# Kernel optimization log

Measured on AMD Instinct MI355X. Metric: run time of the kernel, lower is better.

## Reference

```python
import jax, jax.numpy as jnp
import numpy as np
from jax import lax

B, C, V, F, K = 4, 4, 262144, 64, 100
EMA_THETA = 0.9
TAU = 0.1


def setup_inputs() -> dict:
    key = jax.random.key(0)
    k1, k2, k3 = jax.random.split(key, 3)
    proba = jax.random.uniform(k1, (B, C, V), dtype=jnp.float32)
    y = jax.random.randint(k2, (B, C, V), 0, 2, dtype=jnp.int32)
    embeddings = jax.random.normal(k3, (B, F, V), dtype=jnp.float32)
    avg_repr = jnp.zeros((1, C, F), dtype=jnp.float32)  # EMA buffer
    return {"proba": proba, "y": y, "embeddings": embeddings, "avg_repr": avg_repr}


def reference(proba, y, embeddings, avg_repr):
    # --- update average class representation (EMA over masked voxel means) ---
    mask = (y > 0).astype(embeddings.dtype)                      # [B,C,V]
    class_sum = jnp.einsum("bfv,bcv->cf", embeddings, mask)      # [C,F]
    count = jnp.sum(mask, axis=(0, 2))                           # [C]
    mean = class_sum / jnp.maximum(count, 1.0)[:, None]          # [C,F]
    # original: avg*(1-theta) + mean*theta, only for classes with >0 voxels
    avg_new = jnp.where(
        (count > 0)[None, :, None],
        avg_repr * (1.0 - EMA_THETA) + mean[None] * EMA_THETA,
        avg_repr,
    )                                                            # [1,C,F]

    # --- hard example mining: top-k of prod over class probs per voxel ---
    weights = jnp.prod(proba, axis=1)                            # [B,V]
    _, idx = lax.top_k(weights, K)                               # [B,K]
    emb_bvF = jnp.transpose(embeddings, (0, 2, 1))               # [B,V,F]
    he = jnp.take_along_axis(emb_bvF, idx[..., None], axis=1)    # [B,K,F]
    c_map = jnp.argmax(y, axis=1)                                # [B,V] class per voxel
    he_class = jnp.take_along_axis(c_map, idx, axis=1)           # [B,K]

    # --- l_anco: original loop returns on first iteration (class i=0) ---
    i = 0
    nar = avg_new[0, 1:, :]                                      # [C-1,F] (delete class 0)
    # num/(num/neg_den) == neg_den, so out = -log(neg_den) per the source math
    neg_den = jnp.sum(jnp.exp(he[:, :, None, :] * nar[None, None] / TAU), axis=2)  # [B,K,F]
    out = -jnp.log(neg_den)                                      # [B,K,F]
    sel = (he_class == i).astype(out.dtype)                      # [B,K]
    loss = jnp.sum(out, axis=-1) * sel                           # [B,K], masked instead of boolean-select
    return loss
```

## Files before the change

kernel.cpp:

```cpp
#include <hip/hip_runtime.h>

#define B_ 4
#define C_ 4
#define V_ 262144
#define F_ 64
#define K_ 100
#define THETA 0.9f
#define TAU_ 0.1f

typedef unsigned long long ull;


__global__ __launch_bounds__(256) void k_prep(const int* __restrict__ y,
                                              const float* __restrict__ proba,
                                              unsigned short* __restrict__ mask16,
                                              unsigned* __restrict__ cntp,
                                              unsigned short* __restrict__ hist1p,
                                              unsigned* __restrict__ wbits,
                                              float* __restrict__ cs2) {
    __shared__ unsigned lh[256];
    __shared__ unsigned wc[4][2];
    int blk = blockIdx.x;
    int tid = threadIdx.x;
    int wave = tid >> 6, lane = tid & 63;
    int b = blk >> 8;
    int i4 = ((blk & 255) << 8) | tid;

    lh[tid] = 0u;
    if (blk < 8) cs2[(blk << 8) | tid] = 0.f;
    __syncthreads();

    const int4* y1 = (const int4*)(y + ((size_t)(b * C_ + 1)) * V_);
    const int4* y2 = (const int4*)(y + ((size_t)(b * C_ + 2)) * V_);
    const int4* y3 = (const int4*)(y + ((size_t)(b * C_ + 3)) * V_);
    int4 yb = y1[i4], yc = y2[i4], yd = y3[i4];

    unsigned n0 = ((unsigned)(yb.x > 0) << 1) | ((unsigned)(yc.x > 0) << 2) | ((unsigned)(yd.x > 0) << 3);
    unsigned n1 = ((unsigned)(yb.y > 0) << 1) | ((unsigned)(yc.y > 0) << 2) | ((unsigned)(yd.y > 0) << 3);
    unsigned n2 = ((unsigned)(yb.z > 0) << 1) | ((unsigned)(yc.z > 0) << 2) | ((unsigned)(yd.z > 0) << 3);
    unsigned n3 = ((unsigned)(yb.w > 0) << 1) | ((unsigned)(yc.w > 0) << 2) | ((unsigned)(yd.w > 0) << 3);
    mask16[(size_t)b * (V_ / 4) + i4] = (unsigned short)(n0 | (n1 << 4) | (n2 << 8) | (n3 << 12));

    unsigned p12 = ((unsigned)(yb.x > 0) + (yb.y > 0) + (yb.z > 0) + (yb.w > 0))
                 | (((unsigned)(yc.x > 0) + (yc.y > 0) + (yc.z > 0) + (yc.w > 0)) << 16);
    unsigned p3 = (unsigned)(yd.x > 0) + (yd.y > 0) + (yd.z > 0) + (yd.w > 0);
    #pragma unroll
    for (int o = 1; o < 64; o <<= 1) {
        p12 += __shfl_xor(p12, o, 64);
        p3 += __shfl_xor(p3, o, 64);
    }
    if (lane == 0) { wc[wave][0] = p12; wc[wave][1] = p3; }

    const float* p0 = proba + (size_t)(b * C_) * V_;
    float4 qa = ((const float4*)p0)[i4];
    float4 qb = ((const float4*)(p0 + V_))[i4];
    float4 qc = ((const float4*)(p0 + 2 * V_))[i4];
    float4 qd = ((const float4*)(p0 + 3 * V_))[i4];
    uint4 wb;
    wb.x = __float_as_uint(((qa.x * qb.x) * qc.x) * qd.x);
    wb.y = __float_as_uint(((qa.y * qb.y) * qc.y) * qd.y);
    wb.z = __float_as_uint(((qa.z * qb.z) * qc.z) * qd.z);
    wb.w = __float_as_uint(((qa.w * qb.w) * qc.w) * qd.w);
    ((uint4*)wbits)[(size_t)b * (V_ / 4) + i4] = wb;
    atomicAdd(&lh[wb.x >> 24], 1u);
    atomicAdd(&lh[wb.y >> 24], 1u);
    atomicAdd(&lh[wb.z >> 24], 1u);
    atomicAdd(&lh[wb.w >> 24], 1u);
    __syncthreads();

    hist1p[(blk << 8) | tid] = (unsigned short)lh[tid];
    if (tid == 0) {
        unsigned q12 = wc[0][0] + wc[1][0] + wc[2][0] + wc[3][0];
        unsigned q3 = wc[0][1] + wc[1][1] + wc[2][1] + wc[3][1];
        unsigned* o4 = cntp + (blk << 2);
        o4[0] = 0u; o4[1] = q12 & 0xFFFFu;
        o4[2] = q12 >> 16; o4[3] = q3;
    }
}

__global__ __launch_bounds__(256) void k_class_sum(const float* __restrict__ emb,
                                                   const unsigned short* __restrict__ mask16,
                                                   float* __restrict__ cs2,
                                                   const unsigned short* __restrict__ hist1p,
                                                   const unsigned* __restrict__ cntp,
                                                   unsigned* __restrict__ ctrl1,
                                                   float* __restrict__ cnt) {
    __shared__ unsigned short smask[16384];
    __shared__ unsigned bins[256];
    __shared__ float wsum[4][4];
    int blk = blockIdx.x;
    int tid = threadIdx.x;
    int wave = tid >> 6, lane = tid & 63;

    if (blk >= 1024) {
        if (blk < 1028) {
            int b = blk - 1024;
            unsigned s = 0;
            for (int c = 0; c < 256; ++c)
                s += hist1p[(((b << 8) | c) << 8) | tid];
            bins[tid] = s;
            __syncthreads();
            if (wave == 0) {
                int binbase = 255 - 4 * lane;
                unsigned c0 = bins[binbase], c1 = bins[binbase - 1], c2 = bins[binbase - 2], c3 = bins[binbase - 3];
                unsigned cnt4 = c0 + c1 + c2 + c3;
                unsigned pref = cnt4;
                #pragma unroll
                for (int o = 1; o < 64; o <<= 1) {
                    unsigned u = __shfl_up(pref, o, 64);
                    if (lane >= o) pref += u;
                }
                unsigned above = pref - cnt4;
                unsigned t = above;
                int found = -1; unsigned nab = 0;
                if (t + c0 >= K_)                { found = binbase;     nab = t; }
                else if (t + c0 + c1 >= K_)      { found = binbase - 1; nab = t + c0; }
                else if (t + c0 + c1 + c2 >= K_) { found = binbase - 2; nab = t + c0 + c1; }
                else if (t + cnt4 >= K_)         { found = binbase - 3; nab = t + c0 + c1 + c2; }
                if (found >= 0 && above < K_) {
                    ctrl1[b * 2] = (unsigned)found;
                    ctrl1[b * 2 + 1] = nab;
                }
            }
        } else if (wave == 0) {
            unsigned s1 = 0, s2 = 0, s3 = 0;
            #pragma unroll
            for (int r = 0; r < 16; ++r) {
                uint4 p = ((const uint4*)cntp)[(r << 6) | lane];
                s1 += p.y; s2 += p.z; s3 += p.w;
            }
            #pragma unroll
            for (int o = 1; o < 64; o <<= 1) {
                s1 += __shfl_xor(s1, o, 64);
                s2 += __shfl_xor(s2, o, 64);
                s3 += __shfl_xor(s3, o, 64);
            }
            if (lane == 0) {
                cnt[0] = 0.f; cnt[1] = (float)s1;
                cnt[2] = (float)s2; cnt[3] = (float)s3;
            }
        }
        return;
    }

    int s = blk & 3;
    int f = (blk >> 2) & 63;
    int b = blk >> 8;

    {
        const uint4* msrc = (const uint4*)(mask16 + (size_t)b * (V_ / 4) + (s << 14));
        uint4* mdst = (uint4*)smask;
        #pragma unroll
        for (int i = 0; i < 8; ++i) mdst[(i << 8) | tid] = msrc[(i << 8) | tid];
    }
    __syncthreads();

    const float4* ep = (const float4*)emb + ((size_t)((b << 6) | f)) * (V_ / 4) + ((size_t)s << 14);

    float a1 = 0.f, a2 = 0.f, a3 = 0.f;
    for (int o = 0; o < 8; ++o) {
        float4 e[8];
        unsigned mm[8];
        #pragma unroll
        for (int i = 0; i < 8; ++i) e[i] = ep[(((o << 3) | i) << 8) | tid];
        #pragma unroll
        for (int i = 0; i < 8; ++i) mm[i] = smask[(((o << 3) | i) << 8) | tid];
        #pragma unroll
        for (int i = 0; i < 8; ++i) {
            unsigned m = mm[i];
            float4 ev = e[i];
            a1 += ((m >>  1) & 1u ? ev.x : 0.f) + ((m >>  5) & 1u ? ev.y : 0.f)
                + ((m >>  9) & 1u ? ev.z : 0.f) + ((m >> 13) & 1u ? ev.w : 0.f);
            a2 += ((m >>  2) & 1u ? ev.x : 0.f) + ((m >>  6) & 1u ? ev.y : 0.f)
                + ((m >> 10) & 1u ? ev.z : 0.f) + ((m >> 14) & 1u ? ev.w : 0.f);
            a3 += ((m >>  3) & 1u ? ev.x : 0.f) + ((m >>  7) & 1u ? ev.y : 0.f)
                + ((m >> 11) & 1u ? ev.z : 0.f) + ((m >> 15) & 1u ? ev.w : 0.f);
        }
    }
    #pragma unroll
    for (int o = 1; o < 64; o <<= 1) {
        a1 += __shfl_xor(a1, o, 64);
        a2 += __shfl_xor(a2, o, 64);
        a3 += __shfl_xor(a3, o, 64);
    }
    if (lane == 0) { wsum[wave][0] = a1; wsum[wave][1] = a2; wsum[wave][2] = a3; }
    __syncthreads();
    if (tid < 3) {
        float v = wsum[0][tid] + wsum[1][tid] + wsum[2][tid] + wsum[3][tid];
        atomicAdd(&cs2[((blk & 7) << 8) | ((tid + 1) << 6) | f], v);
    }
}

__global__ __launch_bounds__(256) void k_collect(const unsigned* __restrict__ wbits,
                                                 const unsigned* __restrict__ ctrl1,
                                                 unsigned* __restrict__ cntblk,
                                                 unsigned* __restrict__ sbits,
                                                 unsigned* __restrict__ sidx) {
    __shared__ unsigned lcnt;
    int blk = blockIdx.x;
    int b = blk >> 8;
    int cb = blk & 255;
    int tid = threadIdx.x;
    if (tid == 0) lcnt = 0u;
    __syncthreads();
    unsigned T1 = ctrl1[b * 2];
    int base = cb << 10;
    int sb = ((b << 8) | cb) << 6;
    #pragma unroll
    for (int it = 0; it < 4; ++it) {
        int v = base + tid + (it << 8);
        unsigned bits = wbits[(size_t)b * V_ + v];
        if ((bits >> 24) >= T1) {
            unsigned pos = atomicAdd(&lcnt, 1u);
            if (pos < 64u) { sbits[sb | pos] = bits; sidx[sb | pos] = (unsigned)v; }
        }
    }
    __syncthreads();
    if (tid == 0) cntblk[(b << 8) | cb] = (lcnt < 64u) ? lcnt : 64u;
}

#define XSTEP(kk_, k_, j_) { \
    _Pragma("unroll") \
    for (int r = 0; r < 8; ++r) { \
        ull o = __shfl_xor(kk_[r], (j_) >> 3, 64); \
        int p = (lane << 3) | r; \
        bool keepmax = (((p & (k_)) == 0) == ((p & (j_)) == 0)); \
        kk_[r] = (keepmax == (kk_[r] > o)) ? kk_[r] : o; \
    } }
#define LSTEP(kk_, k_, j_) { \
    _Pragma("unroll") \
    for (int r = 0; r < 8; ++r) { \
        if (!(r & (j_))) { \
            int p = (lane << 3) | r; \
            bool up = ((p & (k_)) == 0); \
            ull a = kk_[r], c = kk_[r | (j_)]; \
            ull mx = a > c ? a : c, mn = a > c ? c : a; \
            kk_[r] = up ? mx : mn; \
            kk_[r | (j_)] = up ? mn : mx; \
        } \
    } }

__global__ __launch_bounds__(256) void k_select(const unsigned* __restrict__ ctrl1,
                                                const unsigned* __restrict__ cntblk,
                                                const unsigned* __restrict__ sbits,
                                                const unsigned* __restrict__ sidx,
                                                unsigned* __restrict__ idxout) {
    __shared__ unsigned hist[256];
    __shared__ ull keys[512];
    __shared__ unsigned P16s, fcnt;
    int b = blockIdx.x;
    int tid = threadIdx.x;
    int wave = tid >> 6, lane = tid & 63;
    unsigned T1 = ctrl1[b * 2];
    unsigned nab = ctrl1[b * 2 + 1];

    hist[tid] = 0u;
    keys[tid] = 0ull;
    keys[tid + 256] = 0ull;
    if (tid == 0) fcnt = 0u;
    __syncthreads();

    int c = (int)cntblk[(b << 8) | tid];
    int sb = ((b << 8) | tid) << 6;
    for (int i = 0; i < c; ++i) {
        unsigned bits = sbits[sb | i];
        if ((bits >> 24) == T1) atomicAdd(&hist[(bits >> 16) & 0xFF], 1u);
    }
    __syncthreads();

    if (wave == 0) {
        int binbase = 255 - 4 * lane;
        unsigned c0 = hist[binbase], c1 = hist[binbase - 1], c2 = hist[binbase - 2], c3 = hist[binbase - 3];
        unsigned cnt4 = c0 + c1 + c2 + c3;
        unsigned pref = cnt4;
        #pragma unroll
        for (int o = 1; o < 64; o <<= 1) {
            unsigned u = __shfl_up(pref, o, 64);
            if (lane >= o) pref += u;
        }
        unsigned above = nab + pref - cnt4;
        unsigned t = above;
        int found = -1;
        if (t + c0 >= K_)                { found = binbase;     }
        else if (t + c0 + c1 >= K_)      { found = binbase - 1; }
        else if (t + c0 + c1 + c2 >= K_) { found = binbase - 2; }
        else if (t + cnt4 >= K_)         { found = binbase - 3; }
        if (found >= 0 && above < K_) P16s = (T1 << 8) | (unsigned)found;
    }
    __syncthreads();

    unsigned P16 = P16s;
    for (int i = 0; i < c; ++i) {
        unsigned bits = sbits[sb | i];
        if ((bits >> 16) >= P16) {
            unsigned pos = atomicAdd(&fcnt, 1u);
            if (pos < 512u) keys[pos] = ((ull)bits << 32) | (unsigned)(~sidx[sb | i]);
        }
    }
    __syncthreads();

    if (wave == 0) {
        ull kk[8];
        #pragma unroll
        for (int r = 0; r < 8; ++r) kk[r] = keys[(lane << 3) | r];
        LSTEP(kk, 2, 1)
        LSTEP(kk, 4, 2) LSTEP(kk, 4, 1)
        LSTEP(kk, 8, 4) LSTEP(kk, 8, 2) LSTEP(kk, 8, 1)
        XSTEP(kk, 16, 8) LSTEP(kk, 16, 4) LSTEP(kk, 16, 2) LSTEP(kk, 16, 1)
        XSTEP(kk, 32, 16) XSTEP(kk, 32, 8) LSTEP(kk, 32, 4) LSTEP(kk, 32, 2) LSTEP(kk, 32, 1)
        XSTEP(kk, 64, 32) XSTEP(kk, 64, 16) XSTEP(kk, 64, 8) LSTEP(kk, 64, 4) LSTEP(kk, 64, 2) LSTEP(kk, 64, 1)
        XSTEP(kk, 128, 64) XSTEP(kk, 128, 32) XSTEP(kk, 128, 16) XSTEP(kk, 128, 8) LSTEP(kk, 128, 4) LSTEP(kk, 128, 2) LSTEP(kk, 128, 1)
        XSTEP(kk, 256, 128) XSTEP(kk, 256, 64) XSTEP(kk, 256, 32) XSTEP(kk, 256, 16) XSTEP(kk, 256, 8) LSTEP(kk, 256, 4) LSTEP(kk, 256, 2) LSTEP(kk, 256, 1)
        XSTEP(kk, 512, 256) XSTEP(kk, 512, 128) XSTEP(kk, 512, 64) XSTEP(kk, 512, 32) XSTEP(kk, 512, 16) XSTEP(kk, 512, 8) LSTEP(kk, 512, 4) LSTEP(kk, 512, 2) LSTEP(kk, 512, 1)
        #pragma unroll
        for (int r = 0; r < 8; ++r) {
            int p = (lane << 3) | r;
            if (p < K_) idxout[b * K_ + p] = ~(unsigned)(kk[r] & 0xFFFFFFFFull);
        }
    }
}

__global__ __launch_bounds__(64) void k_final(const float* __restrict__ emb,
                                              const int* __restrict__ y,
                                              const float* __restrict__ avg,
                                              const float* __restrict__ cs2,
                                              const float* __restrict__ cnt,
                                              const unsigned* __restrict__ idxout,
                                              float* __restrict__ out) {
    int blk = blockIdx.x;
    int b = blk / K_;
    int k = blk % K_;
    int lane = threadIdx.x;
    unsigned v = idxout[b * K_ + k];

    float e = emb[((size_t)(b * F_ + lane)) * V_ + v];

    int y0v = y[((size_t)(b * C_ + 0)) * V_ + v];
    int y1v = y[((size_t)(b * C_ + 1)) * V_ + v];
    int y2v = y[((size_t)(b * C_ + 2)) * V_ + v];
    int y3v = y[((size_t)(b * C_ + 3)) * V_ + v];
    int cm = (y0v > 0) ? 0 : ((y1v > 0) ? 1 : ((y2v > 0) ? 2 : ((y3v > 0) ? 3 : 0)));
    float sel = (cm == 0) ? 1.f : 0.f;

    float t = e / TAU_;
    float ssum = 0.f;
    #pragma unroll
    for (int c = 1; c < 4; ++c) {
        float cc = cnt[c];
        float csum = 0.f;
        #pragma unroll
        for (int rep = 0; rep < 8; ++rep) csum += cs2[(rep << 8) | (c << 6) | lane];
        float mean = csum / fmaxf(cc, 1.f);
        float av = avg[c * F_ + lane];
        float nar = (cc > 0.f) ? (av * (1.f - THETA) + mean * THETA) : av;
        ssum += expf(t * nar);
    }
    float term = -logf(ssum);
    #pragma unroll
    for (int o = 32; o > 0; o >>= 1) term += __shfl_down(term, o, 64);
    if (lane == 0) out[b * K_ + k] = term * sel;
}

extern "C" void kernel_launch(void* const* d_in, const int* in_sizes, int n_in,
                              void* d_out, int out_size, void* d_ws, size_t ws_size,
                              hipStream_t stream) {
    const float* proba = (const float*)d_in[0];
    const int* y = (const int*)d_in[1];
    const float* emb = (const float*)d_in[2];
    const float* avg = (const float*)d_in[3];
    float* out = (float*)d_out;

    char* ws = (char*)d_ws;
    float* cs2 = (float*)(ws + 0);
    float* cnt = (float*)(ws + 8192);
    unsigned* ctrl1 = (unsigned*)(ws + 8208);
    unsigned* idxout = (unsigned*)(ws + 8320);
    unsigned* cntp = (unsigned*)(ws + 147456);
    unsigned* cntblk = (unsigned*)(ws + 147456);
    unsigned short* hist1p = (unsigned short*)(ws + 163840);
    unsigned* sbits = (unsigned*)(ws + 163840);
    unsigned* sidx = (unsigned*)(ws + 425984);
    unsigned short* mask16 = (unsigned short*)(ws + 688128);
    unsigned* wbits = (unsigned*)(ws + 1212416);

    k_prep<<<B_ * 256, 256, 0, stream>>>(y, proba, mask16, cntp, hist1p, wbits, cs2);
    k_class_sum<<<1029, 256, 0, stream>>>(emb, mask16, cs2, hist1p, cntp, ctrl1, cnt);
    k_collect<<<B_ * 256, 256, 0, stream>>>(wbits, ctrl1, cntblk, sbits, sidx);
    k_select<<<B_, 256, 0, stream>>>(ctrl1, cntblk, sbits, sidx, idxout);
    k_final<<<B_ * K_, 64, 0, stream>>>(emb, y, avg, cs2, cnt, idxout, out);
}
```

Baseline: 79.06 us.

## Fuse final loss into top-k select kernel and schedule control blocks first

The per-(b,k) final loss kernel is folded into the select kernel. Each of the 4 blocks keeps its top-100 indices in shared memory, and its waves compute 25 losses each with batched gathers, which removes one kernel launch and the idxout round trip. The class_sum kernel's threshold/count control blocks move to the lowest block indices so they get scheduled early, and their histogram loop is unrolled. The cost is that the final stage now runs on only 4 blocks instead of 400, so more serial work falls on each block.

```diff
diff --git a/kernel.cpp b/kernel.cpp
--- a/kernel.cpp
+++ b/kernel.cpp
@@ -92,10 +92,11 @@
     int tid = threadIdx.x;
     int wave = tid >> 6, lane = tid & 63;
 
-    if (blk >= 1024) {
-        if (blk < 1028) {
-            int b = blk - 1024;
+    if (blk < 5) {
+        if (blk < 4) {
+            int b = blk;
             unsigned s = 0;
+            #pragma unroll 8
             for (int c = 0; c < 256; ++c)
                 s += hist1p[(((b << 8) | c) << 8) | tid];
             bins[tid] = s;
@@ -143,9 +144,10 @@
         return;
     }
 
-    int s = blk & 3;
-    int f = (blk >> 2) & 63;
-    int b = blk >> 8;
+    int sblk = blk - 5;
+    int s = sblk & 3;
+    int f = (sblk >> 2) & 63;
+    int b = sblk >> 8;
 
     {
         const uint4* msrc = (const uint4*)(mask16 + (size_t)b * (V_ / 4) + (s << 14));
@@ -187,7 +189,7 @@
     __syncthreads();
     if (tid < 3) {
         float v = wsum[0][tid] + wsum[1][tid] + wsum[2][tid] + wsum[3][tid];
-        atomicAdd(&cs2[((blk & 7) << 8) | ((tid + 1) << 6) | f], v);
+        atomicAdd(&cs2[((sblk & 7) << 8) | ((tid + 1) << 6) | f], v);
     }
 }
 
@@ -244,9 +246,15 @@
                                                 const unsigned* __restrict__ cntblk,
                                                 const unsigned* __restrict__ sbits,
                                                 const unsigned* __restrict__ sidx,
-                                                unsigned* __restrict__ idxout) {
+                                                const float* __restrict__ emb,
+                                                const int* __restrict__ y,
+                                                const float* __restrict__ avg,
+                                                const float* __restrict__ cs2,
+                                                const float* __restrict__ cnt,
+                                                float* __restrict__ out) {
     __shared__ unsigned hist[256];
     __shared__ ull keys[512];
+    __shared__ unsigned topv[112];
     __shared__ unsigned P16s, fcnt;
     int b = blockIdx.x;
     int tid = threadIdx.x;
@@ -315,50 +323,52 @@
         #pragma unroll
         for (int r = 0; r < 8; ++r) {
             int p = (lane << 3) | r;
-            if (p < K_) idxout[b * K_ + p] = ~(unsigned)(kk[r] & 0xFFFFFFFFull);
-        }
-    }
-}
-
-__global__ __launch_bounds__(64) void k_final(const float* __restrict__ emb,
-                                              const int* __restrict__ y,
-                                              const float* __restrict__ avg,
-                                              const float* __restrict__ cs2,
-                                              const float* __restrict__ cnt,
-                                              const unsigned* __restrict__ idxout,
-                                              float* __restrict__ out) {
-    int blk = blockIdx.x;
-    int b = blk / K_;
-    int k = blk % K_;
-    int lane = threadIdx.x;
-    unsigned v = idxout[b * K_ + k];
-
-    float e = emb[((size_t)(b * F_ + lane)) * V_ + v];
-
-    int y0v = y[((size_t)(b * C_ + 0)) * V_ + v];
-    int y1v = y[((size_t)(b * C_ + 1)) * V_ + v];
-    int y2v = y[((size_t)(b * C_ + 2)) * V_ + v];
-    int y3v = y[((size_t)(b * C_ + 3)) * V_ + v];
-    int cm = (y0v > 0) ? 0 : ((y1v > 0) ? 1 : ((y2v > 0) ? 2 : ((y3v > 0) ? 3 : 0)));
-    float sel = (cm == 0) ? 1.f : 0.f;
-
-    float t = e / TAU_;
-    float ssum = 0.f;
+            if (p < K_) topv[p] = ~(unsigned)(kk[r] & 0xFFFFFFFFull);
+        }
+    }
+    __syncthreads();
+
+    float nar[3];
     #pragma unroll
-    for (int c = 1; c < 4; ++c) {
-        float cc = cnt[c];
+    for (int cc_ = 1; cc_ < 4; ++cc_) {
+        float ccv = cnt[cc_];
         float csum = 0.f;
         #pragma unroll
-        for (int rep = 0; rep < 8; ++rep) csum += cs2[(rep << 8) | (c << 6) | lane];
-        float mean = csum / fmaxf(cc, 1.f);
-        float av = avg[c * F_ + lane];
-        float nar = (cc > 0.f) ? (av * (1.f - THETA) + mean * THETA) : av;
-        ssum += expf(t * nar);
-    }
-    float term = -logf(ssum);
-    #pragma unroll
-    for (int o = 32; o > 0; o >>= 1) term += __shfl_down(term, o, 64);
-    if (lane == 0) out[b * K_ + k] = term * sel;
+        for (int rep = 0; rep < 8; ++rep) csum += cs2[(rep << 8) | (cc_ << 6) | lane];
+        float mean = csum / fmaxf(ccv, 1.f);
+        float av = avg[cc_ * F_ + lane];
+        nar[cc_ - 1] = (ccv > 0.f) ? (av * (1.f - THETA) + mean * THETA) : av;
+    }
+    const float* erow = emb + ((size_t)((b << 6) | lane)) * V_;
+    const int* y0p = y + ((size_t)(b * C_ + 0)) * V_;
+    const int* y1p = y + ((size_t)(b * C_ + 1)) * V_;
+    const int* y2p = y + ((size_t)(b * C_ + 2)) * V_;
+    const int* y3p = y + ((size_t)(b * C_ + 3)) * V_;
+
+    for (int j = 0; j < 5; ++j) {
+        float ee[5];
+        int yv0[5], yv1[5], yv2[5], yv3[5];
+        #pragma unroll
+        for (int i = 0; i < 5; ++i) {
+            unsigned v = topv[wave * 25 + j * 5 + i];
+            ee[i] = erow[v];
+            yv0[i] = y0p[v]; yv1[i] = y1p[v]; yv2[i] = y2p[v]; yv3[i] = y3p[v];
+        }
+        #pragma unroll
+        for (int i = 0; i < 5; ++i) {
+            int k = wave * 25 + j * 5 + i;
+            int cm = (yv0[i] > 0) ? 0 : ((yv1[i] > 0) ? 1 : ((yv2[i] > 0) ? 2 : ((yv3[i] > 0) ? 3 : 0)));
+            float sel = (cm == 0) ? 1.f : 0.f;
+            float t = ee[i] / TAU_;
+            float ssum = 0.f;
+            #pragma unroll
+            for (int cc_ = 0; cc_ < 3; ++cc_) ssum += expf(t * nar[cc_]);
+            float term = -logf(ssum);
+            #pragma unroll
+            for (int o = 32; o > 0; o >>= 1) term += __shfl_down(term, o, 64);
+            if (lane == 0) out[b * K_ + k] = term * sel;
+        }
+    }
 }
 
 extern "C" void kernel_launch(void* const* d_in, const int* in_sizes, int n_in,
@@ -374,7 +384,6 @@
     float* cs2 = (float*)(ws + 0);
     float* cnt = (float*)(ws + 8192);
     unsigned* ctrl1 = (unsigned*)(ws + 8208);
-    unsigned* idxout = (unsigned*)(ws + 8320);
     unsigned* cntp = (unsigned*)(ws + 147456);
     unsigned* cntblk = (unsigned*)(ws + 147456);
     unsigned short* hist1p = (unsigned short*)(ws + 163840);
@@ -386,6 +395,5 @@
     k_prep<<<B_ * 256, 256, 0, stream>>>(y, proba, mask16, cntp, hist1p, wbits, cs2);
     k_class_sum<<<1029, 256, 0, stream>>>(emb, mask16, cs2, hist1p, cntp, ctrl1, cnt);
     k_collect<<<B_ * 256, 256, 0, stream>>>(wbits, ctrl1, cntblk, sbits, sidx);
-    k_select<<<B_, 256, 0, stream>>>(ctrl1, cntblk, sbits, sidx, idxout);
-    k_final<<<B_ * K_, 64, 0, stream>>>(emb, y, avg, cs2, cnt, idxout, out);
-}
+    k_select<<<B_, 256, 0, stream>>>(ctrl1, cntblk, sbits, sidx, emb, y, avg, cs2, cnt, out);
+}
```

Measured after the change: 104.2 us. 31.8% more time.
